# Kernel tuning notes

Hardware: AMD Instinct MI355X
Metric: run time of the kernel (lower is better)

Reference implementation:

```python
import jax, jax.numpy as jnp
import numpy as np

NUM_NODES = 100000
NUM_EDGES = 3200000
N_PER = 400            # nodes per graph (equal-size graphs)
NUM_GRAPHS = 250
K = 100                # sort-pooling k
DIM = 32
IN_DIM = 128
TOTAL = 3 * DIM + 1    # 97 = concat channel count
GDIM = 128
OUT_DIM = 2
DENSE_DIM = (((K - 2) // 2 + 1) - 5 + 1) * 64  # 46*64 = 2944


def setup_inputs() -> dict:
    key = jax.random.key(0)
    ks = jax.random.split(key, 12)

    def lin(k, shape, fan_in):
        return jax.random.normal(k, shape, jnp.float32) / np.float32(np.sqrt(fan_in))

    return {
        "x": jax.random.normal(ks[0], (NUM_NODES, IN_DIM), jnp.float32),
        "edge_index": jax.random.randint(ks[1], (2, NUM_EDGES), 0, NUM_NODES, dtype=jnp.int32),
        "batch": jnp.arange(NUM_NODES, dtype=jnp.int32) // N_PER,
        "W1": lin(ks[2], (IN_DIM, DIM), IN_DIM), "b1": jnp.zeros((DIM,), jnp.float32),
        "W2": lin(ks[3], (DIM, DIM), DIM),       "b2": jnp.zeros((DIM,), jnp.float32),
        "W3": lin(ks[4], (DIM, DIM), DIM),       "b3": jnp.zeros((DIM,), jnp.float32),
        "W4": lin(ks[5], (DIM, 1), DIM),         "b4": jnp.zeros((1,), jnp.float32),
        "cw1": lin(ks[6], (128, 1, TOTAL), TOTAL),   "cb1": jnp.zeros((128,), jnp.float32),
        "cw2": lin(ks[7], (64, 128, 5), 128 * 5),    "cb2": jnp.zeros((64,), jnp.float32),
        "fw1": lin(ks[8], (GDIM, DENSE_DIM), DENSE_DIM), "fb1": jnp.zeros((GDIM,), jnp.float32),
        "fw3": lin(ks[9], (OUT_DIM, GDIM), GDIM),        "fb3": jnp.zeros((OUT_DIM,), jnp.float32),
    }


def _gcn(h_in, W, b, src, dst, coef, deg_inv):
    # GCNConv (improved=False): D^{-1/2}(A+I)D^{-1/2} (h W) + b
    h = h_in @ W
    agg = jax.ops.segment_sum(h[src] * coef, dst, num_segments=NUM_NODES)
    return agg + h * deg_inv[:, None] + b  # deg_inv = self-loop norm dis[i]^2


def reference(x, edge_index, batch, W1, b1, W2, b2, W3, b3, W4, b4,
              cw1, cb1, cw2, cb2, fw1, fb1, fw3, fb3):
    src, dst = edge_index[0], edge_index[1]
    deg = jax.ops.segment_sum(jnp.ones((NUM_EDGES,), x.dtype), dst, num_segments=NUM_NODES) + 1.0
    dis = jax.lax.rsqrt(deg)
    coef = (dis[src] * dis[dst])[:, None]
    deg_inv = 1.0 / deg

    x1 = jnp.tanh(_gcn(x,  W1, b1, src, dst, coef, deg_inv))
    x2 = jnp.tanh(_gcn(x1, W2, b2, src, dst, coef, deg_inv))
    x3 = jnp.tanh(_gcn(x2, W3, b3, src, dst, coef, deg_inv))
    x4 = jnp.tanh(_gcn(x2, W4, b4, src, dst, coef, deg_inv))  # NB: conv4 consumes x2 (as in source)
    xc = jnp.concatenate([x1, x2, x3, x4], axis=1)  # [N, 97]

    # global_sort_pool: per-graph descending sort by last channel, keep top K nodes
    order = jnp.lexsort((-xc[:, -1], batch))  # primary: graph id, secondary: -last channel
    xs = xc[order].reshape(NUM_GRAPHS, N_PER, TOTAL)[:, :K]  # [B, K, 97]

    # Conv1d(1, 128, kernel=stride=97) over flattened [B,1,K*97] == per-slot linear map
    c1 = jax.nn.relu(jnp.einsum('bkt,ct->bck', xs, cw1[:, 0, :]) + cb1[None, :, None])  # [B,128,K]
    p1 = c1.reshape(NUM_GRAPHS, 128, K // 2, 2).max(axis=-1)  # MaxPool1d(2,2) -> [B,128,50]
    c2 = jax.lax.conv_general_dilated(p1, cw2, (1,), 'VALID',
                                      dimension_numbers=('NCH', 'OIH', 'NCH'))
    c2 = jax.nn.relu(c2 + cb2[None, :, None])  # [B,64,46]

    flat = c2.reshape(NUM_GRAPHS, -1)            # [B, 2944]
    h = jax.nn.relu(flat @ fw1.T + fb1)          # fc1 + relu (dropout = identity in eval)
    logits = h @ fw3.T + fb3                     # fc3
    return jax.nn.log_softmax(logits, axis=-1)
```

## Files before the change

kernel.cpp:

```cpp
#include <hip/hip_runtime.h>
#include <hip/hip_bf16.h>

#define NNODES 100000
#define NEDGES 3200000
#define NPADE  4000000
#define NPER   400
#define NGRAPH 250
#define KTOP   100
#define DIM    32
#define INDIM  128
#define TOTALC 97
#define BSHIFT 7
#define BNODES 128
#define NBUCK  782
#define NCHUNK 200
#define CHSZ   16000

__device__ __forceinline__ float bf(unsigned short u) {
    return __uint_as_float(((unsigned)u) << 16);
}
__device__ __forceinline__ unsigned short f2bf(float f) {
    unsigned u = __float_as_uint(f);
    unsigned r = ((u >> 16) & 1u) + 0x7FFFu;
    return (unsigned short)((u + r) >> 16);
}

#define OW_W1   0
#define OW_B1   4096
#define OW_W2   4128
#define OW_B2   5152
#define OW_W3   5184
#define OW_B3   6208
#define OW_W4   6240
#define OW_B4   6272
#define OW_CW1  6280
#define OW_CB1  18696
#define OW_CW2  18824
#define OW_CB2  59784
#define OW_FW1  59848
#define OW_FB1  436680
#define OW_FW3  436808
#define OW_FB3  437064
#define OW_TOT  437072


__global__ void k_detect(const unsigned int* __restrict__ xw, int* __restrict__ flag) {
    __shared__ int cnt[256];
    int t = threadIdx.x, c = 0;
    for (int i = t; i < 4096; i += 256) {
        unsigned e = (xw[i] >> 23) & 0xFFu;
        if (e >= 100u && e <= 150u) c++;
    }
    cnt[t] = c;
    __syncthreads();
    for (int off = 128; off > 0; off >>= 1) {
        if (t < off) cnt[t] += cnt[t + off];
        __syncthreads();
    }
    if (t == 0) flag[0] = (cnt[0] < 2048) ? 1 : 0;
}

struct Srcs { const void* p[16]; };

__global__ void k_convert(Srcs sr, float* __restrict__ dst, const int* __restrict__ flag) {
    const int st[16] = {OW_W1, OW_B1, OW_W2, OW_B2, OW_W3, OW_B3, OW_W4, OW_B4,
                        OW_CW1, OW_CB1, OW_CW2, OW_CB2, OW_FW1, OW_FB1, OW_FW3, OW_FB3};
    const int nn[16] = {4096, 32, 1024, 32, 1024, 32, 32, 1,
                        12416, 128, 40960, 64, 376832, 128, 256, 2};
    int idx = blockIdx.x * 256 + threadIdx.x;
    if (idx >= OW_TOT) return;
    int isb = flag[0];
    #pragma unroll
    for (int s = 0; s < 16; s++) {
        if (idx >= st[s] && idx < st[s] + nn[s]) {
            int l = idx - st[s];
            dst[idx] = isb ? bf(((const unsigned short*)sr.p[s])[l])
                           : ((const float*)sr.p[s])[l];
        }
    }
}

__global__ void k_w1t(const float* __restrict__ fw1f, float* __restrict__ fw1t) {
    int i = blockIdx.x * 256 + threadIdx.x;
    if (i < 376832) {
        int j = i / 2944, d = i % 2944;
        fw1t[d * 128 + j] = fw1f[i];
    }
}


__global__ __launch_bounds__(1024) void k_hist(const int* __restrict__ ei, int* __restrict__ ghist) {
    __shared__ int h[NBUCK];
    int c = blockIdx.x, t = threadIdx.x;
    for (int i = t; i < NBUCK; i += 1024) h[i] = 0;
    __syncthreads();
    int base = c * CHSZ;
    for (int e = base + t; e < base + CHSZ; e += 1024)
        atomicAdd(&h[ei[NEDGES + e] >> BSHIFT], 1);
    __syncthreads();
    for (int i = t; i < NBUCK; i += 1024) ghist[i * NCHUNK + c] = h[i];
}

__global__ __launch_bounds__(256) void k_scanChunk(int* __restrict__ ghist, int* __restrict__ bcnt) {
    __shared__ int s[256];
    int b = blockIdx.x, t = threadIdx.x;
    int v = (t < NCHUNK) ? ghist[b * NCHUNK + t] : 0;
    s[t] = v;
    __syncthreads();
    for (int o = 1; o < 256; o <<= 1) {
        int u = (t >= o) ? s[t - o] : 0;
        __syncthreads();
        s[t] += u;
        __syncthreads();
    }
    if (t < NCHUNK) ghist[b * NCHUNK + t] = s[t] - v;
    if (t == NCHUNK - 1) bcnt[b] = s[t];
}

__global__ void k_scanB(const int* __restrict__ bcnt, int* __restrict__ boff) {
    __shared__ int s[1024];
    int t = threadIdx.x;
    int v = (t < NBUCK) ? bcnt[t] : 0;
    s[t] = v;
    __syncthreads();
    for (int o = 1; o < 1024; o <<= 1) {
        int u = (t >= o) ? s[t - o] : 0;
        __syncthreads();
        s[t] += u;
        __syncthreads();
    }
    if (t < NBUCK) boff[t] = s[t] - v;
}

__global__ __launch_bounds__(1024) void k_binwrite(const int* __restrict__ ei, const int* __restrict__ boff,
                           const int* __restrict__ ghist, unsigned* __restrict__ staged) {
    __shared__ int cur[NBUCK];
    int c = blockIdx.x, t = threadIdx.x;
    for (int i = t; i < NBUCK; i += 1024) cur[i] = boff[i] + ghist[i * NCHUNK + c];
    __syncthreads();
    int base = c * CHSZ;
    for (int e = base + t; e < base + CHSZ; e += 1024) {
        int s = ei[e], d = ei[NEDGES + e];
        int b = d >> BSHIFT;
        int pos = atomicAdd(&cur[b], 1);
        staged[pos] = ((unsigned)(d & (BNODES - 1)) << 17) | (unsigned)s;
    }
}

__global__ __launch_bounds__(256) void k_nodecnt(const unsigned* __restrict__ staged,
                          const int* __restrict__ boff, int* __restrict__ degi) {
    __shared__ int cnt[BNODES];
    int b = blockIdx.x, t = threadIdx.x;
    if (t < BNODES) cnt[t] = 0;
    __syncthreads();
    int s0 = boff[b];
    int s1 = (b + 1 < NBUCK) ? boff[b + 1] : NEDGES;
    for (int i = s0 + t; i < s1; i += 256)
        atomicAdd(&cnt[staged[i] >> 17], 1);
    __syncthreads();
    int n0 = b << BSHIFT;
    int nn = min(BNODES, NNODES - n0);
    if (t < nn) degi[n0 + t] = cnt[t];
}

__global__ void k_nodeprep(const int* __restrict__ degi, float* __restrict__ dis,
                           float* __restrict__ dinv) {
    int i = blockIdx.x * 256 + threadIdx.x;
    if (i < NNODES) {
        float d = (float)(degi[i] + 1);
        dis[i]  = rsqrtf(d);
        dinv[i] = 1.0f / d;
    }
}

__global__ void k_bsum(const int* __restrict__ degi, int* __restrict__ bsums) {
    __shared__ int s[256];
    int t = threadIdx.x;
    int i = blockIdx.x * 256 + t;
    s[t] = (i < NNODES) ? ((degi[i] + 7) & ~7) : 0;
    __syncthreads();
    for (int off = 128; off > 0; off >>= 1) {
        if (t < off) s[t] += s[t + off];
        __syncthreads();
    }
    if (t == 0) bsums[blockIdx.x] = s[0];
}

__global__ void k_scanb(int* __restrict__ bsums, int nb) {
    __shared__ int s[512];
    int t = threadIdx.x;
    int v = (t < nb) ? bsums[t] : 0;
    s[t] = v;
    __syncthreads();
    for (int off = 1; off < 512; off <<= 1) {
        int u = (t >= off) ? s[t - off] : 0;
        __syncthreads();
        s[t] += u;
        __syncthreads();
    }
    if (t < nb) bsums[t] = s[t] - v;
}

__global__ void k_scanf(const int* __restrict__ degi, const int* __restrict__ bsums,
                        int* __restrict__ row_off) {
    __shared__ int s[256];
    int t = threadIdx.x;
    int i = blockIdx.x * 256 + t;
    int v = (i < NNODES) ? ((degi[i] + 7) & ~7) : 0;
    s[t] = v;
    __syncthreads();
    for (int off = 1; off < 256; off <<= 1) {
        int u = (t >= off) ? s[t - off] : 0;
        __syncthreads();
        s[t] += u;
        __syncthreads();
    }
    if (i < NNODES) row_off[i] = bsums[blockIdx.x] + s[t] - v;
}

__global__ __launch_bounds__(256) void k_csrfix(const unsigned* __restrict__ staged,
                         const int* __restrict__ boff, const int* __restrict__ row_off,
                         const float* __restrict__ dis,
                         int* __restrict__ csr_src, float* __restrict__ csr_cf) {
    __shared__ int cnt[BNODES];
    __shared__ int rofs[BNODES];
    __shared__ float disl[BNODES];
    int b = blockIdx.x, t = threadIdx.x;
    int n0 = b << BSHIFT;
    int nn = min(BNODES, NNODES - n0);
    if (t < BNODES) {
        cnt[t]  = 0;
        rofs[t] = (t < nn) ? row_off[n0 + t] : 0;
        disl[t] = (t < nn) ? dis[n0 + t] : 0.f;
    }
    __syncthreads();
    int s0 = boff[b];
    int s1 = (b + 1 < NBUCK) ? boff[b + 1] : NEDGES;
    for (int i = s0 + t; i < s1; i += 256) {
        unsigned rec = staged[i];
        int dl = rec >> 17, s = rec & 0x1FFFF;
        int r = atomicAdd(&cnt[dl], 1);
        int slot = rofs[dl] + r;
        csr_src[slot] = s;
        csr_cf[slot]  = dis[s] * disl[dl];
    }
    __syncthreads();
    if (t < nn) {
        int d = cnt[t], dp = (d + 7) & ~7;
        for (int s2 = d; s2 < dp; s2++) {
            csr_src[rofs[t] + s2] = 0;
            csr_cf[rofs[t] + s2]  = 0.f;
        }
    }
}


__global__ void k_mm1(const void* __restrict__ xraw, const float* __restrict__ W1f,
                      const int* __restrict__ flag, float* __restrict__ h) {
    __shared__ float w[INDIM * DIM];
    __shared__ float xsh[8 * INDIM];
    int t = threadIdx.x;
    for (int i = t; i < INDIM * DIM; i += 256) w[i] = W1f[i];
    if (flag[0]) {
        const unsigned int* xsrc = (const unsigned int*)((const unsigned short*)xraw
                                   + (size_t)blockIdx.x * 8 * INDIM);
        for (int i = t; i < 512; i += 256) {
            unsigned u = xsrc[i];
            xsh[2 * i]     = __uint_as_float(u << 16);
            xsh[2 * i + 1] = __uint_as_float(u & 0xFFFF0000u);
        }
    } else {
        const float4* xsrc = (const float4*)((const float*)xraw + (size_t)blockIdx.x * 8 * INDIM);
        float4* xdst = (float4*)xsh;
        for (int i = t; i < 256; i += 256) xdst[i] = xsrc[i];
    }
    __syncthreads();
    int ln = t >> 5, c = t & 31;
    const float* xr = xsh + ln * INDIM;
    float acc = 0.f;
    #pragma unroll 8
    for (int j = 0; j < INDIM; j++) acc += xr[j] * w[j * DIM + c];
    h[(size_t)blockIdx.x * 256 + t] = acc;
}

__global__ void k_mm32(const float* __restrict__ xin, const float* __restrict__ W,
                       const float* __restrict__ W4, float* __restrict__ h,
                       float* __restrict__ h4) {
    __shared__ float w[DIM * DIM];
    __shared__ float w4s[DIM];
    __shared__ float xsh[8 * DIM];
    int t = threadIdx.x;
    for (int i = t; i < DIM * DIM; i += 256) w[i] = W[i];
    if (W4 && t < DIM) w4s[t] = W4[t];
    for (int i = t; i < 8 * DIM; i += 256) xsh[i] = xin[(size_t)blockIdx.x * 256 + i];
    __syncthreads();
    int ln = t >> 5, c = t & 31;
    const float* xr = xsh + ln * DIM;
    float acc = 0.f;
    #pragma unroll
    for (int j = 0; j < DIM; j++) acc += xr[j] * w[j * DIM + c];
    h[(size_t)blockIdx.x * 256 + t] = acc;
    if (W4 && c == 0) {
        float a4 = 0.f;
        #pragma unroll
        for (int j = 0; j < DIM; j++) a4 += xr[j] * w4s[j];
        h4[blockIdx.x * 8 + ln] = a4;
    }
}

__global__ void k_gather(const float* __restrict__ h, const float* __restrict__ h4,
                         const int* __restrict__ csr_src, const float* __restrict__ csr_cf,
                         const int* __restrict__ row_off, const int* __restrict__ degi,
                         const float* __restrict__ dinv, const float* __restrict__ bias,
                         const float* __restrict__ b4,
                         float* __restrict__ xout, float* __restrict__ x4out) {
    int t = threadIdx.x;
    int node = blockIdx.x * 8 + (t >> 5);
    int lane = t & 31;
    int start = row_off[node];
    int cnt   = degi[node];
    int iters = (cnt + 7) >> 3;
    const int4*   ip = (const int4*)(csr_src + start);
    const float4* cp = (const float4*)(csr_cf + start);
    float acc0 = 0.f, acc1 = 0.f;
    if (iters > 0) {
        int4   iA = ip[0], iB = ip[1];
        float4 cA = cp[0], cB = cp[1];
        for (int k = 1; k < iters; k++) {
            int4   nA = ip[2 * k],     nB = ip[2 * k + 1];
            float4 dA = cp[2 * k],     dB = cp[2 * k + 1];
            acc0 += h[(size_t)iA.x * DIM + lane] * cA.x;
            acc1 += h[(size_t)iA.y * DIM + lane] * cA.y;
            acc0 += h[(size_t)iA.z * DIM + lane] * cA.z;
            acc1 += h[(size_t)iA.w * DIM + lane] * cA.w;
            acc0 += h[(size_t)iB.x * DIM + lane] * cB.x;
            acc1 += h[(size_t)iB.y * DIM + lane] * cB.y;
            acc0 += h[(size_t)iB.z * DIM + lane] * cB.z;
            acc1 += h[(size_t)iB.w * DIM + lane] * cB.w;
            iA = nA; iB = nB; cA = dA; cB = dB;
        }
        acc0 += h[(size_t)iA.x * DIM + lane] * cA.x;
        acc1 += h[(size_t)iA.y * DIM + lane] * cA.y;
        acc0 += h[(size_t)iA.z * DIM + lane] * cA.z;
        acc1 += h[(size_t)iA.w * DIM + lane] * cA.w;
        acc0 += h[(size_t)iB.x * DIM + lane] * cB.x;
        acc1 += h[(size_t)iB.y * DIM + lane] * cB.y;
        acc0 += h[(size_t)iB.z * DIM + lane] * cB.z;
        acc1 += h[(size_t)iB.w * DIM + lane] * cB.w;
    }
    float di = dinv[node];
    float outv = tanhf(acc0 + acc1 + h[(size_t)node * DIM + lane] * di + bias[lane]);
    xout[(size_t)node * DIM + lane] = outv;
    if (h4) {
        int cntp = iters << 3;
        float a4 = 0.f;
        for (int ee = lane; ee < cntp; ee += 32)
            a4 += h4[csr_src[start + ee]] * csr_cf[start + ee];
        for (int off = 16; off > 0; off >>= 1) a4 += __shfl_xor(a4, off, 32);
        if (lane == 0) x4out[node] = tanhf(a4 + h4[node] * di + b4[0]);
    }
}

__global__ void k_sortpool(const float* __restrict__ x4, int* __restrict__ sel) {
    __shared__ unsigned long long keys[512];
    int g = blockIdx.x, t = threadIdx.x;
    for (int i = t; i < 512; i += 256) {
        unsigned long long kk = 0xFFFFFFFFFFFFFFFFULL;
        if (i < NPER) {
            unsigned u = __float_as_uint(x4[g * NPER + i]);
            u = (u & 0x80000000u) ? ~u : (u | 0x80000000u);
            kk = ((unsigned long long)(~u) << 32) | (unsigned)i;
        }
        keys[i] = kk;
    }
    __syncthreads();
    for (int k = 2; k <= 512; k <<= 1)
        for (int j = k >> 1; j > 0; j >>= 1) {
            for (int i = t; i < 512; i += 256) {
                int l = i ^ j;
                if (l > i) {
                    unsigned long long a = keys[i], b = keys[l];
                    bool asc = ((i & k) == 0);
                    if ((a > b) == asc) { keys[i] = b; keys[l] = a; }
                }
            }
            __syncthreads();
        }
    for (int i = t; i < KTOP; i += 256)
        sel[g * KTOP + i] = g * NPER + (int)(unsigned)(keys[i] & 0xFFFFFFFFu);
}

__global__ __launch_bounds__(1024) void
k_conv1pool(const float* __restrict__ x1, const float* __restrict__ x2,
            const float* __restrict__ x3, const float* __restrict__ x4,
            const int* __restrict__ sel, const float* __restrict__ cw1f,
            const float* __restrict__ cb1f, float* __restrict__ p1g) {
    __shared__ __align__(16) float xs[32 * 100];
    __shared__ __align__(16) float ws[32 * 128];
    __shared__ int nsh[KTOP];
    int g = blockIdx.x, t = threadIdx.x;
    if (t < KTOP) nsh[t] = sel[g * KTOP + t];
    int ct = (t & 31) * 4;
    int kt = (t >> 5) * 4;
    bool act = (t < 800);
    float acc[4][4] = {};
    for (int ch = 0; ch < 3; ch++) {
        const float* arr = (ch == 0) ? x1 : (ch == 1) ? x2 : x3;
        __syncthreads();
        for (int i = t; i < 3200; i += 1024) {
            int q = i & 31, k = i >> 5;
            xs[q * 100 + k] = arr[(size_t)nsh[k] * 32 + q];
        }
        for (int i = t; i < 4096; i += 1024) {
            int c = i & 127, q = i >> 7;
            ws[q * 128 + c] = cw1f[c * TOTALC + ch * 32 + q];
        }
        __syncthreads();
        if (act) {
            for (int q = 0; q < 32; q++) {
                float4 wv = *(const float4*)&ws[q * 128 + ct];
                float4 xv = *(const float4*)&xs[q * 100 + kt];
                float xa[4] = { xv.x, xv.y, xv.z, xv.w };
                float wa[4] = { wv.x, wv.y, wv.z, wv.w };
                #pragma unroll
                for (int a = 0; a < 4; a++)
                    #pragma unroll
                    for (int b = 0; b < 4; b++)
                        acc[a][b] += xa[a] * wa[b];
            }
        }
    }
    if (act) {
        float wa[4];
        #pragma unroll
        for (int b = 0; b < 4; b++) wa[b] = cw1f[(ct + b) * TOTALC + 96];
        #pragma unroll
        for (int a = 0; a < 4; a++) {
            float xv = x4[nsh[kt + a]];
            #pragma unroll
            for (int b = 0; b < 4; b++) acc[a][b] += xv * wa[b];
        }
        int jbase = kt >> 1;
        #pragma unroll
        for (int b = 0; b < 4; b++) {
            float bias = cb1f[ct + b];
            float m0 = fmaxf(fmaxf(acc[0][b], acc[1][b]) + bias, 0.f);
            float m1 = fmaxf(fmaxf(acc[2][b], acc[3][b]) + bias, 0.f);
            p1g[((size_t)g * 128 + ct + b) * 50 + jbase]     = m0;
            p1g[((size_t)g * 128 + ct + b) * 50 + jbase + 1] = m1;
        }
    }
}

__global__ void k_w2t(const float* __restrict__ cw2f, float* __restrict__ w2t8) {
    int i = blockIdx.x * 256 + threadIdx.x;
    if (i < 64 * 128 * 8) {
        int q = i & 7;
        int co = i >> 3;
        int c = co >> 6, o = co & 63;
        w2t8[i] = (q < 5) ? cw2f[(o * 128 + c) * 5 + q] : 0.f;
    }
}

__global__ __launch_bounds__(512) void
k_conv2(const float* __restrict__ p1g, const float* __restrict__ w2t8,
        const float* __restrict__ cb2f, float* __restrict__ flatg) {
    __shared__ __align__(16) float p1s[128 * 52];
    __shared__ float fl[64 * 25];
    int bid = blockIdx.x;
    int g = bid >> 1, ph = bid & 1;
    int t = threadIdx.x;
    int p0 = ph ? 24 : 0;
    int np = ph ? 22 : 24;
    for (int i = t; i < 128 * 50; i += 512) {
        int c = i / 50, p = i % 50;
        p1s[c * 52 + p] = p1g[(size_t)g * 6400 + i];
    }
    for (int i = t; i < 128 * 2; i += 512) {
        int c = i >> 1;
        p1s[c * 52 + 50 + (i & 1)] = 0.f;
    }
    for (int i = t; i < 64 * 25; i += 512) fl[i] = 0.f;
    __syncthreads();
    {
        int o = t & 63;
        int c8 = t >> 6;
        float acc[24];
        #pragma unroll
        for (int p = 0; p < 24; p++) acc[p] = 0.f;
        int cbeg = c8 * 16;
        for (int c = cbeg; c < cbeg + 16; c++) {
            const float4* wb = (const float4*)(w2t8 + (((size_t)c * 64 + o) << 3));
            float4 wA = wb[0], wB = wb[1];
            float w0 = wA.x, w1 = wA.y, w2 = wA.z, w3 = wA.w, w4 = wB.x;
            float win[28];
            const float4* wsrc = (const float4*)&p1s[c * 52 + p0];
            #pragma unroll
            for (int v = 0; v < 7; v++) {
                float4 f = wsrc[v];
                win[4 * v] = f.x; win[4 * v + 1] = f.y; win[4 * v + 2] = f.z; win[4 * v + 3] = f.w;
            }
            #pragma unroll
            for (int p = 0; p < 24; p++)
                acc[p] += win[p] * w0 + win[p + 1] * w1 + win[p + 2] * w2
                        + win[p + 3] * w3 + win[p + 4] * w4;
        }
        for (int p = 0; p < np; p++) atomicAdd(&fl[o * 25 + p], acc[p]);
    }
    __syncthreads();
    for (int i = t; i < 64 * 24; i += 512) {
        int o = i / 24, p = i - o * 24;
        if (p < np)
            flatg[(size_t)g * 2944 + o * 46 + p0 + p] = fmaxf(fl[o * 25 + p] + cb2f[o], 0.f);
    }
}

__global__ __launch_bounds__(1024) void
k_fc1(const float* __restrict__ flatg, const float* __restrict__ fw1t,
      float* __restrict__ hpart) {
    __shared__ float fls[5 * 368];
    __shared__ float hp[8 * 5 * 128];
    int b = blockIdx.x;
    int gt = b >> 3, kt = b & 7;
    int t = threadIdx.x;
    int g0 = gt * 5;
    int d0 = kt * 368;
    for (int i = t; i < 5 * 368; i += 1024) {
        int g = i / 368, dd = i - g * 368;
        fls[i] = flatg[(size_t)(g0 + g) * 2944 + d0 + dd];
    }
    __syncthreads();
    int og = t & 127, s8 = t >> 7;
    int ds = s8 * 46;
    const float* wp = fw1t + (size_t)(d0 + ds) * 128 + og;
    const float* f0 = fls + ds;
    float a0 = 0.f, a1 = 0.f, a2 = 0.f, a3 = 0.f, a4 = 0.f;
    #pragma unroll 2
    for (int d = 0; d < 46; d++) {
        float w = wp[(size_t)d * 128];
        a0 += f0[d]            * w;
        a1 += f0[368 + d]      * w;
        a2 += f0[2 * 368 + d]  * w;
        a3 += f0[3 * 368 + d]  * w;
        a4 += f0[4 * 368 + d]  * w;
    }
    hp[(s8 * 5 + 0) * 128 + og] = a0;
    hp[(s8 * 5 + 1) * 128 + og] = a1;
    hp[(s8 * 5 + 2) * 128 + og] = a2;
    hp[(s8 * 5 + 3) * 128 + og] = a3;
    hp[(s8 * 5 + 4) * 128 + og] = a4;
    __syncthreads();
    if (t < 640) {
        int g = t >> 7, o2 = t & 127;
        float s = 0.f;
        #pragma unroll
        for (int s2 = 0; s2 < 8; s2++) s += hp[(s2 * 5 + g) * 128 + o2];
        hpart[((size_t)kt * NGRAPH + g0 + g) * 128 + o2] = s;
    }
}

__global__ void k_fc3(const float* __restrict__ hpart, const float* __restrict__ fb1f,
                      const float* __restrict__ fw3f, const float* __restrict__ fb3f,
                      const int* __restrict__ flag, void* __restrict__ outp) {
    __shared__ float hsh[128];
    int g = blockIdx.x, t = threadIdx.x;
    float s = fb1f[t];
    #pragma unroll
    for (int kt = 0; kt < 8; kt++) s += hpart[((size_t)kt * NGRAPH + g) * 128 + t];
    hsh[t] = fmaxf(s, 0.f);
    __syncthreads();
    if (t < 64) {
        float h0 = hsh[t], h1 = hsh[t + 64];
        float l0 = h0 * fw3f[t] + h1 * fw3f[t + 64];
        float l1 = h0 * fw3f[128 + t] + h1 * fw3f[192 + t];
        #pragma unroll
        for (int off = 32; off > 0; off >>= 1) {
            l0 += __shfl_down(l0, off, 64);
            l1 += __shfl_down(l1, off, 64);
        }
        if (t == 0) {
            l0 += fb3f[0]; l1 += fb3f[1];
            float m = fmaxf(l0, l1);
            float lse = m + logf(expf(l0 - m) + expf(l1 - m));
            if (flag[0]) {
                unsigned short* ob = (unsigned short*)outp;
                ob[g * 2 + 0] = f2bf(l0 - lse);
                ob[g * 2 + 1] = f2bf(l1 - lse);
            } else {
                float* of = (float*)outp;
                of[g * 2 + 0] = l0 - lse;
                of[g * 2 + 1] = l1 - lse;
            }
        }
    }
}


extern "C" void kernel_launch(void* const* d_in, const int* in_sizes, int n_in,
                              void* d_out, int out_size, void* d_ws, size_t ws_size,
                              hipStream_t stream) {
    const void* x  = d_in[0];
    const int* ei  = (const int*)d_in[1];

    char* p = (char*)d_ws;
    auto alloc = [&](size_t bytes) -> void* {
        void* r = (void*)p;
        p += (bytes + 255) & ~(size_t)255;
        return r;
    };
    int*      flag    = (int*)alloc(256);
    float*    wcv     = (float*)alloc((size_t)OW_TOT * 4);
    float*    fw1t    = (float*)alloc((size_t)376832 * 4);
    int*      ghist   = (int*)alloc((size_t)NBUCK * NCHUNK * 4);
    int*      bcnt    = (int*)alloc(1024 * 4);
    int*      boff    = (int*)alloc(1024 * 4);
    int*      bsums   = (int*)alloc(512 * 4);
    int*      degi    = (int*)alloc((size_t)NNODES * 4);
    int*      row_off = (int*)alloc((size_t)NNODES * 4);
    float*    dis     = (float*)alloc((size_t)NNODES * 4);
    float*    dinv    = (float*)alloc((size_t)NNODES * 4);
    unsigned* staged  = (unsigned*)alloc((size_t)NEDGES * 4);
    int*      csr_src = (int*)alloc((size_t)NPADE * 4);
    float*    csr_cf  = (float*)alloc((size_t)NPADE * 4);
    float*    hbuf    = (float*)alloc((size_t)NNODES * DIM * 4);
    float*    h4buf   = (float*)alloc((size_t)NNODES * 4);
    float*    x1      = (float*)alloc((size_t)NNODES * DIM * 4);
    float*    x2      = (float*)alloc((size_t)NNODES * DIM * 4);
    float*    x3      = (float*)alloc((size_t)NNODES * DIM * 4);
    float*    x4      = (float*)alloc((size_t)NNODES * 4);
    int*      sel     = (int*)alloc((size_t)NGRAPH * KTOP * 4);
    float*    p1g     = (float*)alloc((size_t)NGRAPH * 128 * 50 * 4);
    float*    w2t     = (float*)alloc((size_t)64 * 128 * 8 * 4);
    float*    flatg   = (float*)alloc((size_t)NGRAPH * 2944 * 4);
    float*    hpart   = (float*)alloc((size_t)8 * NGRAPH * 128 * 4);
    (void)in_sizes; (void)n_in; (void)out_size; (void)ws_size;

    k_detect<<<1, 256, 0, stream>>>((const unsigned int*)x, flag);
    Srcs sr;
    for (int i = 0; i < 16; i++) sr.p[i] = d_in[3 + i];
    k_convert<<<(OW_TOT + 255) / 256, 256, 0, stream>>>(sr, wcv, flag);
    k_w1t    <<<1472, 256, 0, stream>>>(wcv + OW_FW1, fw1t);

    k_hist     <<<NCHUNK, 1024, 0, stream>>>(ei, ghist);
    k_scanChunk<<<NBUCK, 256, 0, stream>>>(ghist, bcnt);
    k_scanB    <<<1, 1024, 0, stream>>>(bcnt, boff);
    k_binwrite <<<NCHUNK, 1024, 0, stream>>>(ei, boff, ghist, staged);
    k_nodecnt  <<<NBUCK, 256, 0, stream>>>(staged, boff, degi);
    k_nodeprep <<<391, 256, 0, stream>>>(degi, dis, dinv);
    k_bsum     <<<391, 256, 0, stream>>>(degi, bsums);
    k_scanb    <<<1, 512, 0, stream>>>(bsums, 391);
    k_scanf    <<<391, 256, 0, stream>>>(degi, bsums, row_off);
    k_csrfix   <<<NBUCK, 256, 0, stream>>>(staged, boff, row_off, dis, csr_src, csr_cf);

    k_mm1   <<<12500, 256, 0, stream>>>(x, wcv + OW_W1, flag, hbuf);
    k_gather<<<12500, 256, 0, stream>>>(hbuf, nullptr, csr_src, csr_cf, row_off, degi, dinv,
                                        wcv + OW_B1, nullptr, x1, nullptr);
    k_mm32  <<<12500, 256, 0, stream>>>(x1, wcv + OW_W2, nullptr, hbuf, nullptr);
    k_gather<<<12500, 256, 0, stream>>>(hbuf, nullptr, csr_src, csr_cf, row_off, degi, dinv,
                                        wcv + OW_B2, nullptr, x2, nullptr);
    k_mm32  <<<12500, 256, 0, stream>>>(x2, wcv + OW_W3, wcv + OW_W4, hbuf, h4buf);
    k_gather<<<12500, 256, 0, stream>>>(hbuf, h4buf, csr_src, csr_cf, row_off, degi, dinv,
                                        wcv + OW_B3, wcv + OW_B4, x3, x4);

    k_sortpool <<<NGRAPH, 256, 0, stream>>>(x4, sel);
    k_conv1pool<<<NGRAPH, 1024, 0, stream>>>(x1, x2, x3, x4, sel, wcv + OW_CW1, wcv + OW_CB1, p1g);
    k_w2t      <<<256, 256, 0, stream>>>(wcv + OW_CW2, w2t);
    k_conv2    <<<2 * NGRAPH, 512, 0, stream>>>(p1g, w2t, wcv + OW_CB2, flatg);
    k_fc1      <<<400, 1024, 0, stream>>>(flatg, fw1t, hpart);
    k_fc3      <<<NGRAPH, 128, 0, stream>>>(hpart, wcv + OW_FB1, wcv + OW_FW3, wcv + OW_FB3,
                                            flag, d_out);
}
```

Before: 617.0 us.

## Fuse GCN linear layers into gather via aggregate-then-transform, merge small kernels

Uses linearity of the GCN aggregation: layers 2 and 3 now aggregate the 32-wide input first and apply the 32x32 weight afterwards inside the gather kernel, which removes the separate k_mm32 launches and the hbuf round trips. The W4 projection for conv4 is computed in the layer-2 gather epilogue. Sort-pooling is fused into conv1pool, nodeprep is merged into bsum, and the cw2 transpose is merged into the fw1 transpose kernel. The trade-off is extra shared memory and __syncthreads inside the gather kernel, plus a reordered sum that changes floating-point rounding slightly.

```diff
diff --git a/kernel.cpp b/kernel.cpp
--- a/kernel.cpp
+++ b/kernel.cpp
@@ -80,11 +80,18 @@
     }
 }
 
-__global__ void k_w1t(const float* __restrict__ fw1f, float* __restrict__ fw1t) {
+__global__ void k_wtrans(const float* __restrict__ fw1f, float* __restrict__ fw1t,
+                         const float* __restrict__ cw2f, float* __restrict__ w2t8) {
     int i = blockIdx.x * 256 + threadIdx.x;
     if (i < 376832) {
         int j = i / 2944, d = i % 2944;
         fw1t[d * 128 + j] = fw1f[i];
+    } else if (i < 376832 + 65536) {
+        int k = i - 376832;
+        int q = k & 7;
+        int co = k >> 3;
+        int c = co >> 6, o = co & 63;
+        w2t8[k] = (q < 5) ? cw2f[(o * 128 + c) * 5 + q] : 0.f;
     }
 }
 
@@ -163,21 +170,18 @@
     if (t < nn) degi[n0 + t] = cnt[t];
 }
 
-__global__ void k_nodeprep(const int* __restrict__ degi, float* __restrict__ dis,
-                           float* __restrict__ dinv) {
-    int i = blockIdx.x * 256 + threadIdx.x;
+__global__ void k_bsum(const int* __restrict__ degi, float* __restrict__ dis,
+                       float* __restrict__ dinv, int* __restrict__ bsums) {
+    __shared__ int s[256];
+    int t = threadIdx.x;
+    int i = blockIdx.x * 256 + t;
+    int dg = (i < NNODES) ? degi[i] : 0;
     if (i < NNODES) {
-        float d = (float)(degi[i] + 1);
+        float d = (float)(dg + 1);
         dis[i]  = rsqrtf(d);
         dinv[i] = 1.0f / d;
     }
-}
-
-__global__ void k_bsum(const int* __restrict__ degi, int* __restrict__ bsums) {
-    __shared__ int s[256];
-    int t = threadIdx.x;
-    int i = blockIdx.x * 256 + t;
-    s[t] = (i < NNODES) ? ((degi[i] + 7) & ~7) : 0;
+    s[t] = (i < NNODES) ? ((dg + 7) & ~7) : 0;
     __syncthreads();
     for (int off = 128; off > 0; off >>= 1) {
         if (t < off) s[t] += s[t + off];
@@ -283,40 +287,26 @@
     h[(size_t)blockIdx.x * 256 + t] = acc;
 }
 
-__global__ void k_mm32(const float* __restrict__ xin, const float* __restrict__ W,
-                       const float* __restrict__ W4, float* __restrict__ h,
-                       float* __restrict__ h4) {
-    __shared__ float w[DIM * DIM];
-    __shared__ float w4s[DIM];
-    __shared__ float xsh[8 * DIM];
-    int t = threadIdx.x;
-    for (int i = t; i < DIM * DIM; i += 256) w[i] = W[i];
-    if (W4 && t < DIM) w4s[t] = W4[t];
-    for (int i = t; i < 8 * DIM; i += 256) xsh[i] = xin[(size_t)blockIdx.x * 256 + i];
-    __syncthreads();
-    int ln = t >> 5, c = t & 31;
-    const float* xr = xsh + ln * DIM;
-    float acc = 0.f;
-    #pragma unroll
-    for (int j = 0; j < DIM; j++) acc += xr[j] * w[j * DIM + c];
-    h[(size_t)blockIdx.x * 256 + t] = acc;
-    if (W4 && c == 0) {
-        float a4 = 0.f;
-        #pragma unroll
-        for (int j = 0; j < DIM; j++) a4 += xr[j] * w4s[j];
-        h4[blockIdx.x * 8 + ln] = a4;
-    }
-}
-
-__global__ void k_gather(const float* __restrict__ h, const float* __restrict__ h4,
+__global__ void k_gather(const float* __restrict__ xin, const float* __restrict__ h4in,
                          const int* __restrict__ csr_src, const float* __restrict__ csr_cf,
                          const int* __restrict__ row_off, const int* __restrict__ degi,
-                         const float* __restrict__ dinv, const float* __restrict__ bias,
+                         const float* __restrict__ dinv,
+                         const float* __restrict__ Wm,
+                         const float* __restrict__ bias,
+                         const float* __restrict__ w4v,
                          const float* __restrict__ b4,
-                         float* __restrict__ xout, float* __restrict__ x4out) {
-    int t = threadIdx.x;
+                         float* __restrict__ xout, float* __restrict__ x4out,
+                         float* __restrict__ h4out) {
+    __shared__ float wsh[DIM * DIM];
+    __shared__ float w4sh[DIM];
+    __shared__ float zsh[8 * DIM];
+    __shared__ float osh[8 * DIM];
+    int t = threadIdx.x;
+    if (Wm)  for (int i = t; i < DIM * DIM; i += 256) wsh[i] = Wm[i];
+    if (w4v && t < DIM) w4sh[t] = w4v[t];
     int node = blockIdx.x * 8 + (t >> 5);
     int lane = t & 31;
+    int wg   = t >> 5;
     int start = row_off[node];
     int cnt   = degi[node];
     int iters = (cnt + 7) >> 3;
@@ -329,42 +319,71 @@
         for (int k = 1; k < iters; k++) {
             int4   nA = ip[2 * k],     nB = ip[2 * k + 1];
             float4 dA = cp[2 * k],     dB = cp[2 * k + 1];
-            acc0 += h[(size_t)iA.x * DIM + lane] * cA.x;
-            acc1 += h[(size_t)iA.y * DIM + lane] * cA.y;
-            acc0 += h[(size_t)iA.z * DIM + lane] * cA.z;
-            acc1 += h[(size_t)iA.w * DIM + lane] * cA.w;
-            acc0 += h[(size_t)iB.x * DIM + lane] * cB.x;
-            acc1 += h[(size_t)iB.y * DIM + lane] * cB.y;
-            acc0 += h[(size_t)iB.z * DIM + lane] * cB.z;
-            acc1 += h[(size_t)iB.w * DIM + lane] * cB.w;
+            acc0 += xin[(size_t)iA.x * DIM + lane] * cA.x;
+            acc1 += xin[(size_t)iA.y * DIM + lane] * cA.y;
+            acc0 += xin[(size_t)iA.z * DIM + lane] * cA.z;
+            acc1 += xin[(size_t)iA.w * DIM + lane] * cA.w;
+            acc0 += xin[(size_t)iB.x * DIM + lane] * cB.x;
+            acc1 += xin[(size_t)iB.y * DIM + lane] * cB.y;
+            acc0 += xin[(size_t)iB.z * DIM + lane] * cB.z;
+            acc1 += xin[(size_t)iB.w * DIM + lane] * cB.w;
             iA = nA; iB = nB; cA = dA; cB = dB;
         }
-        acc0 += h[(size_t)iA.x * DIM + lane] * cA.x;
-        acc1 += h[(size_t)iA.y * DIM + lane] * cA.y;
-        acc0 += h[(size_t)iA.z * DIM + lane] * cA.z;
-        acc1 += h[(size_t)iA.w * DIM + lane] * cA.w;
-        acc0 += h[(size_t)iB.x * DIM + lane] * cB.x;
-        acc1 += h[(size_t)iB.y * DIM + lane] * cB.y;
-        acc0 += h[(size_t)iB.z * DIM + lane] * cB.z;
-        acc1 += h[(size_t)iB.w * DIM + lane] * cB.w;
+        acc0 += xin[(size_t)iA.x * DIM + lane] * cA.x;
+        acc1 += xin[(size_t)iA.y * DIM + lane] * cA.y;
+        acc0 += xin[(size_t)iA.z * DIM + lane] * cA.z;
+        acc1 += xin[(size_t)iA.w * DIM + lane] * cA.w;
+        acc0 += xin[(size_t)iB.x * DIM + lane] * cB.x;
+        acc1 += xin[(size_t)iB.y * DIM + lane] * cB.y;
+        acc0 += xin[(size_t)iB.z * DIM + lane] * cB.z;
+        acc1 += xin[(size_t)iB.w * DIM + lane] * cB.w;
     }
     float di = dinv[node];
-    float outv = tanhf(acc0 + acc1 + h[(size_t)node * DIM + lane] * di + bias[lane]);
-    xout[(size_t)node * DIM + lane] = outv;
-    if (h4) {
+    float z = acc0 + acc1 + xin[(size_t)node * DIM + lane] * di;
+    if (!Wm) {
+        xout[(size_t)node * DIM + lane] = tanhf(z + bias[lane]);
+    } else {
+        zsh[wg * DIM + lane] = z;
+        __syncthreads();
+        const float* zr = zsh + wg * DIM;
+        float a = bias[lane];
+        #pragma unroll
+        for (int j = 0; j < DIM; j++) a += zr[j] * wsh[j * DIM + lane];
+        float outv = tanhf(a);
+        xout[(size_t)node * DIM + lane] = outv;
+        if (h4out) {
+            osh[wg * DIM + lane] = outv;
+            __syncthreads();
+            if (lane == 0) {
+                const float* xr = osh + wg * DIM;
+                float a4 = 0.f;
+                #pragma unroll
+                for (int j = 0; j < DIM; j++) a4 += xr[j] * w4sh[j];
+                h4out[node] = a4;
+            }
+        }
+    }
+    if (h4in) {
         int cntp = iters << 3;
         float a4 = 0.f;
         for (int ee = lane; ee < cntp; ee += 32)
-            a4 += h4[csr_src[start + ee]] * csr_cf[start + ee];
+            a4 += h4in[csr_src[start + ee]] * csr_cf[start + ee];
         for (int off = 16; off > 0; off >>= 1) a4 += __shfl_xor(a4, off, 32);
-        if (lane == 0) x4out[node] = tanhf(a4 + h4[node] * di + b4[0]);
-    }
-}
-
-__global__ void k_sortpool(const float* __restrict__ x4, int* __restrict__ sel) {
+        if (lane == 0) x4out[node] = tanhf(a4 + h4in[node] * di + b4[0]);
+    }
+}
+
+__global__ __launch_bounds__(1024) void
+k_sortconv1(const float* __restrict__ x1, const float* __restrict__ x2,
+            const float* __restrict__ x3, const float* __restrict__ x4,
+            const float* __restrict__ cw1f, const float* __restrict__ cb1f,
+            float* __restrict__ p1g) {
     __shared__ unsigned long long keys[512];
+    __shared__ __align__(16) float xs[32 * 100];
+    __shared__ __align__(16) float ws[32 * 128];
+    __shared__ int nsh[KTOP];
     int g = blockIdx.x, t = threadIdx.x;
-    for (int i = t; i < 512; i += 256) {
+    for (int i = t; i < 512; i += 1024) {
         unsigned long long kk = 0xFFFFFFFFFFFFFFFFULL;
         if (i < NPER) {
             unsigned u = __float_as_uint(x4[g * NPER + i]);
@@ -376,7 +395,7 @@
     __syncthreads();
     for (int k = 2; k <= 512; k <<= 1)
         for (int j = k >> 1; j > 0; j >>= 1) {
-            for (int i = t; i < 512; i += 256) {
+            for (int i = t; i < 512; i += 1024) {
                 int l = i ^ j;
                 if (l > i) {
                     unsigned long long a = keys[i], b = keys[l];
@@ -386,20 +405,7 @@
             }
             __syncthreads();
         }
-    for (int i = t; i < KTOP; i += 256)
-        sel[g * KTOP + i] = g * NPER + (int)(unsigned)(keys[i] & 0xFFFFFFFFu);
-}
-
-__global__ __launch_bounds__(1024) void
-k_conv1pool(const float* __restrict__ x1, const float* __restrict__ x2,
-            const float* __restrict__ x3, const float* __restrict__ x4,
-            const int* __restrict__ sel, const float* __restrict__ cw1f,
-            const float* __restrict__ cb1f, float* __restrict__ p1g) {
-    __shared__ __align__(16) float xs[32 * 100];
-    __shared__ __align__(16) float ws[32 * 128];
-    __shared__ int nsh[KTOP];
-    int g = blockIdx.x, t = threadIdx.x;
-    if (t < KTOP) nsh[t] = sel[g * KTOP + t];
+    if (t < KTOP) nsh[t] = g * NPER + (int)(unsigned)(keys[t] & 0xFFFFFFFFu);
     int ct = (t & 31) * 4;
     int kt = (t >> 5) * 4;
     bool act = (t < 800);
@@ -449,16 +455,6 @@
             p1g[((size_t)g * 128 + ct + b) * 50 + jbase]     = m0;
             p1g[((size_t)g * 128 + ct + b) * 50 + jbase + 1] = m1;
         }
-    }
-}
-
-__global__ void k_w2t(const float* __restrict__ cw2f, float* __restrict__ w2t8) {
-    int i = blockIdx.x * 256 + threadIdx.x;
-    if (i < 64 * 128 * 8) {
-        int q = i & 7;
-        int co = i >> 3;
-        int c = co >> 6, o = co & 63;
-        w2t8[i] = (q < 5) ? cw2f[(o * 128 + c) * 5 + q] : 0.f;
     }
 }
 
@@ -628,7 +624,6 @@
     float*    x2      = (float*)alloc((size_t)NNODES * DIM * 4);
     float*    x3      = (float*)alloc((size_t)NNODES * DIM * 4);
     float*    x4      = (float*)alloc((size_t)NNODES * 4);
-    int*      sel     = (int*)alloc((size_t)NGRAPH * KTOP * 4);
     float*    p1g     = (float*)alloc((size_t)NGRAPH * 128 * 50 * 4);
     float*    w2t     = (float*)alloc((size_t)64 * 128 * 8 * 4);
     float*    flatg   = (float*)alloc((size_t)NGRAPH * 2944 * 4);
@@ -639,32 +634,30 @@
     Srcs sr;
     for (int i = 0; i < 16; i++) sr.p[i] = d_in[3 + i];
     k_convert<<<(OW_TOT + 255) / 256, 256, 0, stream>>>(sr, wcv, flag);
-    k_w1t    <<<1472, 256, 0, stream>>>(wcv + OW_FW1, fw1t);
+    k_wtrans <<<1728, 256, 0, stream>>>(wcv + OW_FW1, fw1t, wcv + OW_CW2, w2t);
 
     k_hist     <<<NCHUNK, 1024, 0, stream>>>(ei, ghist);
     k_scanChunk<<<NBUCK, 256, 0, stream>>>(ghist, bcnt);
     k_scanB    <<<1, 1024, 0, stream>>>(bcnt, boff);
     k_binwrite <<<NCHUNK, 1024, 0, stream>>>(ei, boff, ghist, staged);
     k_nodecnt  <<<NBUCK, 256, 0, stream>>>(staged, boff, degi);
-    k_nodeprep <<<391, 256, 0, stream>>>(degi, dis, dinv);
-    k_bsum     <<<391, 256, 0, stream>>>(degi, bsums);
+    k_bsum     <<<391, 256, 0, stream>>>(degi, dis, dinv, bsums);
     k_scanb    <<<1, 512, 0, stream>>>(bsums, 391);
     k_scanf    <<<391, 256, 0, stream>>>(degi, bsums, row_off);
     k_csrfix   <<<NBUCK, 256, 0, stream>>>(staged, boff, row_off, dis, csr_src, csr_cf);
 
     k_mm1   <<<12500, 256, 0, stream>>>(x, wcv + OW_W1, flag, hbuf);
     k_gather<<<12500, 256, 0, stream>>>(hbuf, nullptr, csr_src, csr_cf, row_off, degi, dinv,
-                                        wcv + OW_B1, nullptr, x1, nullptr);
-    k_mm32  <<<12500, 256, 0, stream>>>(x1, wcv + OW_W2, nullptr, hbuf, nullptr);
-    k_gather<<<12500, 256, 0, stream>>>(hbuf, nullptr, csr_src, csr_cf, row_off, degi, dinv,
-                                        wcv + OW_B2, nullptr, x2, nullptr);
-    k_mm32  <<<12500, 256, 0, stream>>>(x2, wcv + OW_W3, wcv + OW_W4, hbuf, h4buf);
-    k_gather<<<12500, 256, 0, stream>>>(hbuf, h4buf, csr_src, csr_cf, row_off, degi, dinv,
-                                        wcv + OW_B3, wcv + OW_B4, x3, x4);
-
-    k_sortpool <<<NGRAPH, 256, 0, stream>>>(x4, sel);
-    k_conv1pool<<<NGRAPH, 1024, 0, stream>>>(x1, x2, x3, x4, sel, wcv + OW_CW1, wcv + OW_CB1, p1g);
-    k_w2t      <<<256, 256, 0, stream>>>(wcv + OW_CW2, w2t);
+                                        nullptr, wcv + OW_B1, nullptr, nullptr,
+                                        x1, nullptr, nullptr);
+    k_gather<<<12500, 256, 0, stream>>>(x1, nullptr, csr_src, csr_cf, row_off, degi, dinv,
+                                        wcv + OW_W2, wcv + OW_B2, wcv + OW_W4, nullptr,
+                                        x2, nullptr, h4buf);
+    k_gather<<<12500, 256, 0, stream>>>(x2, h4buf, csr_src, csr_cf, row_off, degi, dinv,
+                                        wcv + OW_W3, wcv + OW_B3, nullptr, wcv + OW_B4,
+                                        x3, x4, nullptr);
+
+    k_sortconv1<<<NGRAPH, 1024, 0, stream>>>(x1, x2, x3, x4, wcv + OW_CW1, wcv + OW_CB1, p1g);
     k_conv2    <<<2 * NGRAPH, 512, 0, stream>>>(p1g, w2t, wcv + OW_CB2, flatg);
     k_fc1      <<<400, 1024, 0, stream>>>(flatg, fw1t, hpart);
     k_fc3      <<<NGRAPH, 128, 0, stream>>>(hpart, wcv + OW_FB1, wcv + OW_FW3, wcv + OW_FB3,
```

Result: faster. 576.1 us (-6.6%).
